# Kernel tuning notes

Measured on AMD Instinct MI355X. Metric: run time of the kernel, lower is better.

Reference implementation:

```python
import jax, jax.numpy as jnp
import numpy as np

DIM = 512
HEADS = 8
DIM_HEAD = 64
HIDDEN = HEADS * DIM_HEAD
SCALE = DIM_HEAD ** -0.5


def rmsnorm_ch(x, g):
    # F.normalize over channel dim (axis=1), then * g * sqrt(C)
    # x: [b, c, l], g: [c]
    n = jnp.maximum(jnp.linalg.norm(x, axis=1, keepdims=True), 1e-12)
    c = x.shape[1]
    return (x / n) * g[None, :, None] * (c ** 0.5)


def setup_inputs() -> dict:
    key = jax.random.key(0)
    ks = jax.random.split(key, 6)
    b, l = 8, 4096
    x = jax.random.normal(ks[0], (b, DIM, l), dtype=jnp.float32)
    g_in = jnp.ones((DIM,), dtype=jnp.float32)
    # conv1d kernel_size=1 == matmul; kaiming-ish init scale
    w_qkv = jax.random.normal(ks[1], (3 * HIDDEN, DIM), dtype=jnp.float32) * (1.0 / np.sqrt(DIM))
    w_out = jax.random.normal(ks[2], (DIM, HIDDEN), dtype=jnp.float32) * (1.0 / np.sqrt(HIDDEN))
    b_out = jax.random.normal(ks[3], (DIM,), dtype=jnp.float32) * 0.01
    g_out = jnp.ones((DIM,), dtype=jnp.float32)
    return {"x": x, "g_in": g_in, "w_qkv": w_qkv, "w_out": w_out, "b_out": b_out, "g_out": g_out}


def reference(x, g_in, w_qkv, w_out, b_out, g_out):
    b, c, l = x.shape
    residual = x
    xn = rmsnorm_ch(x, g_in)                       # [b, c, l]
    qkv = jnp.einsum('oc,bcl->bol', w_qkv, xn)     # [b, 3*hidden, l]
    q, k, v = jnp.split(qkv, 3, axis=1)            # each [b, hidden, l]
    def to_heads(t):
        return t.reshape(b, HEADS, DIM_HEAD, l)    # [b, h, d, l]
    q, k, v = to_heads(q), to_heads(k), to_heads(v)
    q = jax.nn.softmax(q, axis=2) * SCALE          # softmax over head-dim d
    k = jax.nn.softmax(k, axis=3)                  # softmax over sequence l
    context = jnp.einsum('bhdn,bhen->bhde', k, v)  # [b, h, d, e]
    out = jnp.einsum('bhde,bhdn->bhen', context, q)  # [b, h, e, l]
    out = out.reshape(b, HIDDEN, l)
    o = jnp.einsum('ch,bhl->bcl', w_out, out) + b_out[None, :, None]
    o = rmsnorm_ch(o, g_out)
    return o + residual
```

## Files before the change

kernel.cpp:

```cpp
#include <hip/hip_runtime.h>


#define BB 8
#define CC 512
#define LL 4096
#define HH 8
#define DH 64
#define TC 1536

__device__ __constant__ const float SQRT_C = 22.62741699796952f;
#define SCALE_Q 0.125f

typedef unsigned short bfr_t;
typedef __attribute__((ext_vector_type(8))) short short8;
typedef __attribute__((ext_vector_type(4))) float f32x4;
typedef __attribute__((ext_vector_type(16))) float f32x16;

__device__ __forceinline__ float bf2f(bfr_t v) {
  union { unsigned u; float f; } c; c.u = ((unsigned)v) << 16; return c.f;
}
__device__ __forceinline__ bfr_t f2bf(float f) {
  union { float f; unsigned u; } c; c.f = f;
  unsigned u = c.u + 0x7fffu + ((c.u >> 16) & 1u);
  return (bfr_t)(u >> 16);
}

__device__ __forceinline__ void load_lds16(const bfr_t* g, short* l) {
  __builtin_amdgcn_global_load_lds(
      (const __attribute__((address_space(1))) void*)g,
      (__attribute__((address_space(3))) void*)l, 16, 0, 0);
}

__global__ __launch_bounds__(256) void conv_bf16_2(
    const float* __restrict__ in1, bfr_t* __restrict__ o1, int n1,
    const float* __restrict__ in2, bfr_t* __restrict__ o2, int n2) {
  int i8 = (blockIdx.x * 256 + threadIdx.x) * 8;
  const float* src;
  bfr_t* dst;
  if (i8 < n1) { src = in1 + i8; dst = o1 + i8; }
  else {
    int j8 = i8 - n1;
    if (j8 >= n2) return;
    src = in2 + j8; dst = o2 + j8;
  }
  f32x4 a = *(const f32x4*)src;
  f32x4 b = *(const f32x4*)(src + 4);
  union { short s[8]; f32x4 v; } pk;
#pragma unroll
  for (int u = 0; u < 4; ++u) { pk.s[u] = (short)f2bf(a[u]); pk.s[u + 4] = (short)f2bf(b[u]); }
  *(f32x4*)dst = pk.v;
}

__global__ __launch_bounds__(256) void fused_norm_transpose(
    const float* __restrict__ x, const float* __restrict__ g,
    bfr_t* __restrict__ xt) {
  __shared__ float tile[64][65];
  __shared__ float red[4][64];
  __shared__ float invn_s[64];
  int b = blockIdx.y, l0 = blockIdx.x * 64;
  int t = threadIdx.x, ll = t & 63, cg = t >> 6;
  const float* xb = x + (size_t)b * CC * LL + l0;
  float vals[8][16];
  float ss = 0.f;
#pragma unroll
  for (int ch = 0; ch < 8; ++ch) {
    int c0 = ch * 64;
#pragma unroll
    for (int i = 0; i < 16; ++i) {
      int c = i * 4 + cg;
      float v = xb[(size_t)(c0 + c) * LL + ll];
      vals[ch][i] = v;
      ss += v * v;
    }
  }
  red[cg][ll] = ss;
  __syncthreads();
  if (cg == 0) {
    float s = red[0][ll] + red[1][ll] + red[2][ll] + red[3][ll];
    invn_s[ll] = SQRT_C / fmaxf(sqrtf(s), 1e-12f);
  }
  __syncthreads();
  int lw = t >> 2, ccw = (t & 3) * 16;
  float iv = invn_s[lw];
#pragma unroll
  for (int ch = 0; ch < 8; ++ch) {
    int c0 = ch * 64;
#pragma unroll
    for (int i = 0; i < 16; ++i) tile[i * 4 + cg][ll] = vals[ch][i];
    __syncthreads();
    union { short s[16]; f32x4 v[2]; } pk;
#pragma unroll
    for (int u = 0; u < 16; ++u) {
      int c = ccw + u;
      pk.s[u] = (short)f2bf(tile[c][lw] * g[c0 + c] * iv);
    }
    bfr_t* dst = xt + ((size_t)b * LL + l0 + lw) * CC + c0 + ccw;
    *(f32x4*)dst = pk.v[0];
    *(f32x4*)(dst + 8) = pk.v[1];
    __syncthreads();
  }
}

__global__ __launch_bounds__(256) void gemm_bf16(
    const bfr_t* __restrict__ A, const bfr_t* __restrict__ Bt,
    bfr_t* __restrict__ Cout, const float* __restrict__ bias, int M) {
  const int K = 512;
  __shared__ short As[128 * 64];
  __shared__ short Bs[128 * 64];
  int b = blockIdx.z;
  int m0 = blockIdx.y * 128, n0 = blockIdx.x * 128;
  int t = threadIdx.x, lane = t & 63, wid = t >> 6;
  int wm = wid & 1, wn = wid >> 1;
  int l31 = lane & 31, half = lane >> 5;
  const bfr_t* Bbase = Bt + (size_t)b * LL * K;

  int lrow = lane >> 3;
  int lgran = (lane & 7) ^ lrow;
  const bfr_t* gA[4];
  const bfr_t* gB[4];
  short* lA[4];
  short* lB[4];
#pragma unroll
  for (int u = 0; u < 4; ++u) {
    int ch = wid * 4 + u;
    int row = ch * 8 + lrow;
    gA[u] = A + (size_t)(m0 + row) * K + lgran * 8;
    gB[u] = Bbase + (size_t)(n0 + row) * K + lgran * 8;
    lA[u] = As + ch * 512;
    lB[u] = Bs + ch * 512;
  }

  f32x16 acc[2][2] = {};

  for (int k0 = 0; k0 < K; k0 += 64) {
    __syncthreads();
#pragma unroll
    for (int u = 0; u < 4; ++u) {
      load_lds16(gA[u] + k0, lA[u]);
      load_lds16(gB[u] + k0, lB[u]);
    }
    __syncthreads();
#pragma unroll
    for (int kk = 0; kk < 4; ++kk) {
      short8 a[2], bq[2];
#pragma unroll
      for (int im = 0; im < 2; ++im) {
        int row = wm * 64 + im * 32 + l31;
        int gk = (kk * 2 + half) ^ (row & 7);
        a[im] = *(const short8*)&As[row * 64 + gk * 8];
      }
#pragma unroll
      for (int jn = 0; jn < 2; ++jn) {
        int row = wn * 64 + jn * 32 + l31;
        int gk = (kk * 2 + half) ^ (row & 7);
        bq[jn] = *(const short8*)&Bs[row * 64 + gk * 8];
      }
#pragma unroll
      for (int im = 0; im < 2; ++im)
#pragma unroll
        for (int jn = 0; jn < 2; ++jn)
          acc[im][jn] = __builtin_amdgcn_mfma_f32_32x32x16_bf16(
              a[im], bq[jn], acc[im][jn], 0, 0, 0);
    }
  }

  bfr_t* Cb = Cout + (size_t)b * M * LL;
#pragma unroll
  for (int im = 0; im < 2; ++im) {
#pragma unroll
    for (int reg = 0; reg < 16; ++reg) {
      int row = m0 + wm * 64 + im * 32 + (reg & 3) + 8 * (reg >> 2) + 4 * half;
      float bi = bias ? bias[row] : 0.f;
#pragma unroll
      for (int jn = 0; jn < 2; ++jn) {
        int col = n0 + wn * 64 + jn * 32 + l31;
        Cb[(size_t)row * LL + col] = f2bf(acc[im][jn][reg] + bi);
      }
    }
  }
}

__global__ __launch_bounds__(256) void context_mfma(
    const bfr_t* __restrict__ qkv, float* __restrict__ ctx_p,
    float* __restrict__ ksum_p) {
  __shared__ float red[4][4096];
  int s = blockIdx.x, bh = blockIdx.y;
  int b = bh >> 3, h = bh & 7;
  int t = threadIdx.x, lane = t & 63, wid = t >> 6;
  int quad = lane >> 4, r = lane & 15;
  const bfr_t* kb = qkv + ((size_t)b * TC + 512 + h * 64) * LL;
  const bfr_t* vb = qkv + ((size_t)b * TC + 1024 + h * 64) * LL;
  int n_base = s * 512 + wid * 128;
  f32x4 acc[4][4] = {};
  float ps[4] = {};
#pragma unroll
  for (int ks = 0; ks < 4; ++ks) {
    int n0 = n_base + ks * 32;
    short8 af[4], bf8[4];
#pragma unroll
    for (int i = 0; i < 4; ++i) {
      union { short s[8]; short8 v8; } uk;
      uk.v8 = *(const short8*)&kb[(size_t)(i * 16 + r) * LL + n0 + quad * 8];
#pragma unroll
      for (int jj = 0; jj < 8; ++jj) {
        float e = __expf(bf2f((bfr_t)uk.s[jj]));
        uk.s[jj] = (short)f2bf(e);
        ps[i] += e;
      }
      af[i] = uk.v8;
      bf8[i] = *(const short8*)&vb[(size_t)(i * 16 + r) * LL + n0 + quad * 8];
    }
#pragma unroll
    for (int i = 0; i < 4; ++i)
#pragma unroll
      for (int j = 0; j < 4; ++j)
        acc[i][j] = __builtin_amdgcn_mfma_f32_16x16x32_bf16(af[i], bf8[j],
                                                            acc[i][j], 0, 0, 0);
  }
#pragma unroll
  for (int i = 0; i < 4; ++i) {
    ps[i] += __shfl_xor(ps[i], 16, 64);
    ps[i] += __shfl_xor(ps[i], 32, 64);
  }
  if (quad == 0) {
#pragma unroll
    for (int i = 0; i < 4; ++i) red[wid][i * 16 + r] = ps[i];
  }
  __syncthreads();
  if (t < 64)
    ksum_p[((size_t)bh * 8 + s) * 64 + t] =
        red[0][t] + red[1][t] + red[2][t] + red[3][t];
  __syncthreads();
#pragma unroll
  for (int i = 0; i < 4; ++i)
#pragma unroll
    for (int j = 0; j < 4; ++j)
#pragma unroll
      for (int reg = 0; reg < 4; ++reg)
        red[wid][(i * 16 + quad * 4 + reg) * 64 + j * 16 + r] = acc[i][j][reg];
  __syncthreads();
  float* out = ctx_p + ((size_t)bh * 8 + s) * 4096;
#pragma unroll
  for (int u = 0; u < 16; ++u) {
    int idx = u * 256 + t;
    out[idx] = red[0][idx] + red[1][idx] + red[2][idx] + red[3][idx];
  }
}

__global__ __launch_bounds__(256) void context_reduce(
    const float* __restrict__ ctx_p, const float* __restrict__ ksum_p,
    bfr_t* __restrict__ ctx_bf) {
  __shared__ float zinv[64];
  int bh = blockIdx.x;
  int t = threadIdx.x;
  if (t < 64) {
    float s = 0.f;
#pragma unroll
    for (int s8 = 0; s8 < 8; ++s8) s += ksum_p[((size_t)bh * 8 + s8) * 64 + t];
    zinv[t] = 1.f / s;
  }
  __syncthreads();
#pragma unroll
  for (int i = 0; i < 16; ++i) {
    int idx = i * 256 + t;
    int d = idx >> 6;
    float sum = 0.f;
#pragma unroll
    for (int s = 0; s < 8; ++s) sum += ctx_p[((size_t)bh * 8 + s) * 4096 + idx];
    ctx_bf[(size_t)bh * 4096 + idx] = f2bf(sum * zinv[d]);
  }
}

__global__ __launch_bounds__(256) void apply_fused(
    const bfr_t* __restrict__ qkv, const bfr_t* __restrict__ ctx_bf,
    bfr_t* __restrict__ out_t) {
  int b = blockIdx.z, h = blockIdx.y;
  int t = threadIdx.x, lane = t & 63, wid = t >> 6;
  int quad = lane >> 4, r = lane & 15;
  int n0 = blockIdx.x * 256 + wid * 64;
  const bfr_t* qb = qkv + ((size_t)b * TC + h * 64) * LL;
  const bfr_t* cb = ctx_bf + (size_t)(b * HH + h) * 4096;
  float v[4][16];
  float pm[4];
#pragma unroll
  for (int i = 0; i < 4; ++i) {
    pm[i] = -1e30f;
#pragma unroll
    for (int ks = 0; ks < 2; ++ks)
#pragma unroll
      for (int jj = 0; jj < 8; ++jj) {
        float q = bf2f(qb[(size_t)(ks * 32 + quad * 8 + jj) * LL + n0 + i * 16 + r]);
        v[i][ks * 8 + jj] = q;
        pm[i] = fmaxf(pm[i], q);
      }
  }
#pragma unroll
  for (int i = 0; i < 4; ++i) {
    pm[i] = fmaxf(pm[i], __shfl_xor(pm[i], 16, 64));
    pm[i] = fmaxf(pm[i], __shfl_xor(pm[i], 32, 64));
  }
  float psum[4];
#pragma unroll
  for (int i = 0; i < 4; ++i) {
    float s = 0.f;
#pragma unroll
    for (int u = 0; u < 16; ++u) { v[i][u] = __expf(v[i][u] - pm[i]); s += v[i][u]; }
    psum[i] = s;
  }
#pragma unroll
  for (int i = 0; i < 4; ++i) {
    psum[i] += __shfl_xor(psum[i], 16, 64);
    psum[i] += __shfl_xor(psum[i], 32, 64);
  }
  short8 af[2][4];
#pragma unroll
  for (int i = 0; i < 4; ++i) {
    float sc = SCALE_Q / psum[i];
#pragma unroll
    for (int ks = 0; ks < 2; ++ks) {
      union { short s[8]; short8 v8; } u;
#pragma unroll
      for (int jj = 0; jj < 8; ++jj) u.s[jj] = (short)f2bf(v[i][ks * 8 + jj] * sc);
      af[ks][i] = u.v8;
    }
  }
  short8 bfrag[2][4];
#pragma unroll
  for (int ks = 0; ks < 2; ++ks)
#pragma unroll
    for (int j = 0; j < 4; ++j) {
      union { short s[8]; short8 v8; } u;
#pragma unroll
      for (int jj = 0; jj < 8; ++jj)
        u.s[jj] = (short)cb[(ks * 32 + quad * 8 + jj) * 64 + j * 16 + r];
      bfrag[ks][j] = u.v8;
    }
  f32x4 acc[4][4] = {};
#pragma unroll
  for (int ks = 0; ks < 2; ++ks)
#pragma unroll
    for (int i = 0; i < 4; ++i)
#pragma unroll
      for (int j = 0; j < 4; ++j)
        acc[i][j] = __builtin_amdgcn_mfma_f32_16x16x32_bf16(af[ks][i], bfrag[ks][j],
                                                            acc[i][j], 0, 0, 0);
  bfr_t* dst = out_t + (size_t)b * LL * 512 + h * 64;
#pragma unroll
  for (int i = 0; i < 4; ++i)
#pragma unroll
    for (int reg = 0; reg < 4; ++reg) {
      int row = n0 + i * 16 + quad * 4 + reg;
#pragma unroll
      for (int j = 0; j < 4; ++j)
        dst[(size_t)row * 512 + j * 16 + r] = f2bf(acc[i][j][reg]);
    }
}

__global__ __launch_bounds__(256) void final_norm_res(
    const bfr_t* __restrict__ o, const float* __restrict__ g,
    const float* __restrict__ x, float* __restrict__ out) {
  __shared__ float red[4][64];
  __shared__ float invn[64];
  int b = blockIdx.y, l0 = blockIdx.x * 64;
  int t = threadIdx.x, ll = t & 63, cg = t >> 6;
  const bfr_t* ob = o + (size_t)b * CC * LL + l0 + ll;
  float ss = 0.f;
  for (int c = cg * 128; c < cg * 128 + 128; ++c) {
    float v = bf2f(ob[(size_t)c * LL]);
    ss += v * v;
  }
  red[cg][ll] = ss;
  __syncthreads();
  if (cg == 0) {
    float s = red[0][ll] + red[1][ll] + red[2][ll] + red[3][ll];
    invn[ll] = SQRT_C / fmaxf(sqrtf(s), 1e-12f);
  }
  __syncthreads();
  float iv = invn[ll];
  const float* xb = x + (size_t)b * CC * LL + l0 + ll;
  float* outb = out + (size_t)b * CC * LL + l0 + ll;
  for (int c = cg * 128; c < cg * 128 + 128; ++c) {
    float v = bf2f(ob[(size_t)c * LL]);
    outb[(size_t)c * LL] = v * g[c] * iv + xb[(size_t)c * LL];
  }
}

extern "C" void kernel_launch(void* const* d_in, const int* in_sizes, int n_in,
                              void* d_out, int out_size, void* d_ws,
                              size_t ws_size, hipStream_t stream) {
  const float* x     = (const float*)d_in[0];
  const float* g_in  = (const float*)d_in[1];
  const float* w_qkv = (const float*)d_in[2];
  const float* w_out = (const float*)d_in[3];
  const float* b_out = (const float*)d_in[4];
  const float* g_out = (const float*)d_in[5];
  float* out = (float*)d_out;

  char* ws = (char*)d_ws;
  const size_t off_wqkv  = 0;
  const size_t off_wout  = 1572864;
  const size_t off_ksump = 2097152;
  const size_t off_ctx   = 2260992;
  const size_t off_ctxp  = 3309568;
  const size_t off_xt    = 11698176;
  const size_t off_qkv   = 45252608;
  const size_t ws_need   = 145915904;
  if (ws_size < ws_need) return;

  bfr_t* wqkv_bf = (bfr_t*)(ws + off_wqkv);
  bfr_t* wout_bf = (bfr_t*)(ws + off_wout);
  float* ksum_p  = (float*)(ws + off_ksump);
  bfr_t* ctx_bf  = (bfr_t*)(ws + off_ctx);
  float* ctxp    = (float*)(ws + off_ctxp);
  bfr_t* xt      = (bfr_t*)(ws + off_xt);
  bfr_t* qkv     = (bfr_t*)(ws + off_qkv);
  bfr_t* o_bf    = (bfr_t*)(ws + off_qkv);

  conv_bf16_2<<<dim3((1536 * 512 + 512 * 512) / 8 / 256), 256, 0, stream>>>(
      w_qkv, wqkv_bf, 1536 * 512, w_out, wout_bf, 512 * 512);
  fused_norm_transpose<<<dim3(LL / 64, BB), 256, 0, stream>>>(x, g_in, xt);
  gemm_bf16<<<dim3(LL / 128, TC / 128, BB), 256, 0, stream>>>(wqkv_bf, xt, qkv, nullptr, TC);
  context_mfma<<<dim3(8, BB * HH), 256, 0, stream>>>(qkv, ctxp, ksum_p);
  context_reduce<<<dim3(BB * HH), 256, 0, stream>>>(ctxp, ksum_p, ctx_bf);
  apply_fused<<<dim3(LL / 256, HH, BB), 256, 0, stream>>>(qkv, ctx_bf, xt);
  gemm_bf16<<<dim3(LL / 128, CC / 128, BB), 256, 0, stream>>>(wout_bf, xt, o_bf, b_out, CC);
  final_norm_res<<<dim3(LL / 64, BB), 256, 0, stream>>>(o_bf, g_out, x, out);
}
```

Baseline: 308.9 us.

## Replace 128x128 GEMM with 256x256 double-buffered ping-pong MFMA GEMM

Result: faster. 294.0 us (-4.8%).

```diff
diff --git a/kernel.cpp b/kernel.cpp
--- a/kernel.cpp
+++ b/kernel.cpp
@@ -101,80 +101,136 @@
   }
 }
 
-__global__ __launch_bounds__(256) void gemm_bf16(
+#define NT 8
+
+__device__ __forceinline__ void stage_half(const bfr_t* g, short* l, int wid) {
+  load_lds16(g + (size_t)wid * 8192,        l + wid * 1024);
+  load_lds16(g + (size_t)wid * 8192 + 4096, l + wid * 1024 + 512);
+}
+
+#define CFENCE asm volatile("" ::: "memory")
+#define PHASE_MID()                                          \
+  do { CFENCE; __builtin_amdgcn_s_barrier();                 \
+       asm volatile("s_waitcnt lgkmcnt(0)" ::: "memory");    \
+       __builtin_amdgcn_sched_barrier(0); } while (0)
+#define PHASE_END()                                          \
+  do { CFENCE; __builtin_amdgcn_s_barrier(); CFENCE; } while (0)
+
+#define LOAD_A(QM) do {                                           \
+    const short* ab_ = Ah + (QM) * 4096;                          \
+    _Pragma("unroll") for (int i_ = 0; i_ < 4; ++i_) {            \
+      a_reg[i_ * 2 + 0] = *(const short8*)(ab_ + i_ * 1024 + a_off0); \
+      a_reg[i_ * 2 + 1] = *(const short8*)(ab_ + i_ * 1024 + a_off1); \
+    } } while (0)
+
+#define LOAD_B(QN) do {                                           \
+    const short* bb_ = Bh + (QN) * 2048;                          \
+    _Pragma("unroll") for (int j_ = 0; j_ < 2; ++j_) {            \
+      b_reg[QN][j_ * 2 + 0] = *(const short8*)(bb_ + j_ * 1024 + b_off0); \
+      b_reg[QN][j_ * 2 + 1] = *(const short8*)(bb_ + j_ * 1024 + b_off1); \
+    } } while (0)
+
+#define MMA_Q(QM, QN) do {                                                   \
+    __builtin_amdgcn_s_setprio(1);                                           \
+    _Pragma("unroll") for (int i_ = 0; i_ < 4; ++i_) {                       \
+      _Pragma("unroll") for (int j_ = 0; j_ < 2; ++j_) {                     \
+        acc[(QM) * 4 + i_][(QN) * 2 + j_] =                                  \
+            __builtin_amdgcn_mfma_f32_16x16x32_bf16(                         \
+                a_reg[i_ * 2 + 0], b_reg[QN][j_ * 2 + 0],                    \
+                acc[(QM) * 4 + i_][(QN) * 2 + j_], 0, 0, 0);                 \
+        acc[(QM) * 4 + i_][(QN) * 2 + j_] =                                  \
+            __builtin_amdgcn_mfma_f32_16x16x32_bf16(                         \
+                a_reg[i_ * 2 + 1], b_reg[QN][j_ * 2 + 1],                    \
+                acc[(QM) * 4 + i_][(QN) * 2 + j_], 0, 0, 0);                 \
+      } }                                                                    \
+    __builtin_amdgcn_s_setprio(0); } while (0)
+
+__global__ __launch_bounds__(512, 2) void gemm256(
     const bfr_t* __restrict__ A, const bfr_t* __restrict__ Bt,
     bfr_t* __restrict__ Cout, const float* __restrict__ bias, int M) {
-  const int K = 512;
-  __shared__ short As[128 * 64];
-  __shared__ short Bs[128 * 64];
-  int b = blockIdx.z;
-  int m0 = blockIdx.y * 128, n0 = blockIdx.x * 128;
+  __shared__ short lds[65536];
+  short* As = lds;
+  short* Bs = lds + 32768;
+  int bz = blockIdx.z;
+  int m0 = blockIdx.y * 256, n0 = blockIdx.x * 256;
   int t = threadIdx.x, lane = t & 63, wid = t >> 6;
-  int wm = wid & 1, wn = wid >> 1;
-  int l31 = lane & 31, half = lane >> 5;
-  const bfr_t* Bbase = Bt + (size_t)b * LL * K;
-
-  int lrow = lane >> 3;
-  int lgran = (lane & 7) ^ lrow;
-  const bfr_t* gA[4];
-  const bfr_t* gB[4];
-  short* lA[4];
-  short* lB[4];
-#pragma unroll
-  for (int u = 0; u < 4; ++u) {
-    int ch = wid * 4 + u;
-    int row = ch * 8 + lrow;
-    gA[u] = A + (size_t)(m0 + row) * K + lgran * 8;
-    gB[u] = Bbase + (size_t)(n0 + row) * K + lgran * 8;
-    lA[u] = As + ch * 512;
-    lB[u] = Bs + ch * 512;
-  }
-
-  f32x16 acc[2][2] = {};
-
-  for (int k0 = 0; k0 < K; k0 += 64) {
-    __syncthreads();
-#pragma unroll
-    for (int u = 0; u < 4; ++u) {
-      load_lds16(gA[u] + k0, lA[u]);
-      load_lds16(gB[u] + k0, lB[u]);
-    }
-    __syncthreads();
-#pragma unroll
-    for (int kk = 0; kk < 4; ++kk) {
-      short8 a[2], bq[2];
-#pragma unroll
-      for (int im = 0; im < 2; ++im) {
-        int row = wm * 64 + im * 32 + l31;
-        int gk = (kk * 2 + half) ^ (row & 7);
-        a[im] = *(const short8*)&As[row * 64 + gk * 8];
-      }
-#pragma unroll
-      for (int jn = 0; jn < 2; ++jn) {
-        int row = wn * 64 + jn * 32 + l31;
-        int gk = (kk * 2 + half) ^ (row & 7);
-        bq[jn] = *(const short8*)&Bs[row * 64 + gk * 8];
-      }
-#pragma unroll
-      for (int im = 0; im < 2; ++im)
-#pragma unroll
-        for (int jn = 0; jn < 2; ++jn)
-          acc[im][jn] = __builtin_amdgcn_mfma_f32_32x32x16_bf16(
-              a[im], bq[jn], acc[im][jn], 0, 0, 0);
-    }
-  }
-
-  bfr_t* Cb = Cout + (size_t)b * M * LL;
-#pragma unroll
-  for (int im = 0; im < 2; ++im) {
-#pragma unroll
-    for (int reg = 0; reg < 16; ++reg) {
-      int row = m0 + wm * 64 + im * 32 + (reg & 3) + 8 * (reg >> 2) + 4 * half;
+  int quad = lane >> 4, r16 = lane & 15;
+  int wm = wid >> 2, wn = wid & 3;
+  int soff = (lane >> 3) * 512 + (((lane & 7) ^ (lane >> 3)) * 8);
+  int slot0 = (quad ^ (lane & 7)) * 8;
+  int slot1 = ((4 + quad) ^ (lane & 7)) * 8;
+  int a_off0 = r16 * 64 + slot0, a_off1 = r16 * 64 + slot1;
+  int bb0 = ((wn & 1) * 64 + r16) * 64;
+  int b_off0 = bb0 + slot0, b_off1 = bb0 + slot1;
+
+  const bfr_t* pA0 = A + (size_t)m0 * 512 + soff;
+  const bfr_t* pA1 = pA0 + (size_t)128 * 512;
+  const bfr_t* pB0 = Bt + (size_t)bz * LL * 512 + (size_t)n0 * 512 + soff;
+  const bfr_t* pB1 = pB0 + (size_t)128 * 512;
+
+  f32x4 acc[8][4] = {};
+  short8 a_reg[8];
+  short8 b_reg[2][4];
+
+  stage_half(pA0, As, wid);
+  stage_half(pA1, As + 8192, wid);
+  stage_half(pB0, Bs, wid);
+  stage_half(pB1, Bs + 8192, wid);
+  stage_half(pA0 + 64, As + 16384, wid);
+  stage_half(pA1 + 64, As + 24576, wid);
+  stage_half(pB0 + 64, Bs + 16384, wid);
+  stage_half(pB1 + 64, Bs + 24576, wid);
+  asm volatile("s_waitcnt vmcnt(8)" ::: "memory");
+  CFENCE; __builtin_amdgcn_s_barrier(); CFENCE;
+
+#pragma unroll
+  for (int kt = 0; kt < NT; ++kt) {
+    const int buf = kt & 1;
+    const short* Ah = As + (buf * 2 + wm) * 8192;
+    const short* Bh = Bs + (buf * 2 + (wn >> 1)) * 8192;
+    LOAD_A(0);
+    LOAD_B(0);
+    if (kt >= 1 && kt <= NT - 2)
+      stage_half(pA1 + (kt + 1) * 64, As + (((kt + 1) & 1) * 2 + 1) * 8192, wid);
+    PHASE_MID();
+    MMA_Q(0, 0);
+    PHASE_END();
+    LOAD_B(1);
+    PHASE_MID();
+    MMA_Q(0, 1);
+    PHASE_END();
+    LOAD_A(1);
+    if (kt <= NT - 3)
+      stage_half(pB0 + (kt + 2) * 64, Bs + (buf * 2) * 8192, wid);
+    PHASE_MID();
+    MMA_Q(1, 1);
+    PHASE_END();
+    if (kt <= NT - 3) {
+      stage_half(pB1 + (kt + 2) * 64, Bs + (buf * 2 + 1) * 8192, wid);
+      stage_half(pA0 + (kt + 2) * 64, As + (buf * 2) * 8192, wid);
+    }
+    PHASE_MID();
+    MMA_Q(1, 0);
+    __builtin_amdgcn_sched_barrier(0);
+    if (kt <= NT - 3)      { asm volatile("s_waitcnt vmcnt(6)" ::: "memory"); }
+    else if (kt == NT - 2) { asm volatile("s_waitcnt vmcnt(0)" ::: "memory"); }
+    CFENCE; __builtin_amdgcn_s_barrier(); CFENCE;
+  }
+
+  bfr_t* Cb = Cout + (size_t)bz * M * LL;
+  int crow = m0 + wm * 128 + quad * 4;
+  int ccol = n0 + wn * 64 + r16;
+#pragma unroll
+  for (int am = 0; am < 8; ++am) {
+    int rbase = crow + (am >> 2) * 64 + (am & 3) * 16;
+#pragma unroll
+    for (int reg = 0; reg < 4; ++reg) {
+      int row = rbase + reg;
       float bi = bias ? bias[row] : 0.f;
 #pragma unroll
-      for (int jn = 0; jn < 2; ++jn) {
-        int col = n0 + wn * 64 + jn * 32 + l31;
-        Cb[(size_t)row * LL + col] = f2bf(acc[im][jn][reg] + bi);
+      for (int an = 0; an < 4; ++an) {
+        int col = ccol + (an >> 1) * 32 + (an & 1) * 16;
+        Cb[(size_t)row * LL + col] = f2bf(acc[am][an][reg] + bi);
       }
     }
   }
@@ -419,10 +475,10 @@
   conv_bf16_2<<<dim3((1536 * 512 + 512 * 512) / 8 / 256), 256, 0, stream>>>(
       w_qkv, wqkv_bf, 1536 * 512, w_out, wout_bf, 512 * 512);
   fused_norm_transpose<<<dim3(LL / 64, BB), 256, 0, stream>>>(x, g_in, xt);
-  gemm_bf16<<<dim3(LL / 128, TC / 128, BB), 256, 0, stream>>>(wqkv_bf, xt, qkv, nullptr, TC);
+  gemm256<<<dim3(LL / 256, TC / 256, BB), 512, 0, stream>>>(wqkv_bf, xt, qkv, nullptr, TC);
   context_mfma<<<dim3(8, BB * HH), 256, 0, stream>>>(qkv, ctxp, ksum_p);
   context_reduce<<<dim3(BB * HH), 256, 0, stream>>>(ctxp, ksum_p, ctx_bf);
   apply_fused<<<dim3(LL / 256, HH, BB), 256, 0, stream>>>(qkv, ctx_bf, xt);
-  gemm_bf16<<<dim3(LL / 128, CC / 128, BB), 256, 0, stream>>>(wout_bf, xt, o_bf, b_out, CC);
+  gemm256<<<dim3(LL / 256, CC / 256, BB), 512, 0, stream>>>(wout_bf, xt, o_bf, b_out, CC);
   final_norm_res<<<dim3(LL / 64, BB), 256, 0, stream>>>(o_bf, g_out, x, out);
 }
```
